# Kernel optimization log

Hardware: AMD Instinct MI355X
Metric: run time of the kernel (lower is better)

The kernel has to match this reference:

```python
import jax, jax.numpy as jnp
import numpy as np

BN_EPS = 1e-5


def trilinear_sample(feat, grid):
    """F.grid_sample 5D, mode='bilinear', padding_mode='border', align_corners=True.
    feat: (B,C,D,H,W); grid: (B,N,3) in [-1,1], last dim ordered (x,y,z) -> (W,H,D).
    Returns (B,N,C)."""
    B, C, D, H, W = feat.shape
    # align_corners=True unnormalization; border padding == clamp continuous coord
    x = jnp.clip((grid[..., 0] + 1.0) * 0.5 * (W - 1), 0.0, W - 1)
    y = jnp.clip((grid[..., 1] + 1.0) * 0.5 * (H - 1), 0.0, H - 1)
    z = jnp.clip((grid[..., 2] + 1.0) * 0.5 * (D - 1), 0.0, D - 1)
    x0 = jnp.floor(x).astype(jnp.int32); x1 = jnp.minimum(x0 + 1, W - 1)
    y0 = jnp.floor(y).astype(jnp.int32); y1 = jnp.minimum(y0 + 1, H - 1)
    z0 = jnp.floor(z).astype(jnp.int32); z1 = jnp.minimum(z0 + 1, D - 1)
    wx = (x - x0)[:, None, :]  # (B,1,N)
    wy = (y - y0)[:, None, :]
    wz = (z - z0)[:, None, :]
    flat = feat.reshape(B, C, D * H * W)

    def gather(zi, yi, xi):
        idx = (zi * H + yi) * W + xi            # (B,N)
        return jnp.take_along_axis(flat, idx[:, None, :], axis=2)  # (B,C,N)

    c00 = gather(z0, y0, x0) * (1 - wx) + gather(z0, y0, x1) * wx
    c01 = gather(z0, y1, x0) * (1 - wx) + gather(z0, y1, x1) * wx
    c10 = gather(z1, y0, x0) * (1 - wx) + gather(z1, y0, x1) * wx
    c11 = gather(z1, y1, x0) * (1 - wx) + gather(z1, y1, x1) * wx
    c0 = c00 * (1 - wy) + c01 * wy
    c1 = c10 * (1 - wy) + c11 * wy
    out = c0 * (1 - wz) + c1 * wz               # (B,C,N)
    return out.transpose(0, 2, 1)                # (B,N,C)


def batchnorm(x, gamma, beta, mean, var):
    # inference-mode BatchNorm1d over channel (last) dim
    return (x - mean) * jax.lax.rsqrt(var + BN_EPS) * gamma + beta


def setup_inputs() -> dict:
    key = jax.random.key(0)
    ks = jax.random.split(key, 16)
    B, C, D, H, W = 2, 128, 64, 64, 64
    N = 65536
    h1, h2 = 512, 512
    inp = {
        "dense_features": jax.random.normal(ks[0], (B, C, D, H, W), dtype=jnp.float32),
        "query_points": jax.random.uniform(ks[1], (B, N, 3), dtype=jnp.float32),
        "W1": jax.random.normal(ks[2], (C, h1), dtype=jnp.float32) / np.sqrt(C),
        "b1": jax.random.normal(ks[3], (h1,), dtype=jnp.float32) * 0.01,
        "g1": jax.random.uniform(ks[4], (h1,), dtype=jnp.float32, minval=0.5, maxval=1.5),
        "be1": jax.random.normal(ks[5], (h1,), dtype=jnp.float32) * 0.1,
        "m1": jax.random.normal(ks[6], (h1,), dtype=jnp.float32) * 0.1,
        "v1": jax.random.uniform(ks[7], (h1,), dtype=jnp.float32, minval=0.5, maxval=1.5),
        "W2": jax.random.normal(ks[8], (h1, h2), dtype=jnp.float32) / np.sqrt(h1),
        "b2": jax.random.normal(ks[9], (h2,), dtype=jnp.float32) * 0.01,
        "g2": jax.random.uniform(ks[10], (h2,), dtype=jnp.float32, minval=0.5, maxval=1.5),
        "be2": jax.random.normal(ks[11], (h2,), dtype=jnp.float32) * 0.1,
        "m2": jax.random.normal(ks[12], (h2,), dtype=jnp.float32) * 0.1,
        "v2": jax.random.uniform(ks[13], (h2,), dtype=jnp.float32, minval=0.5, maxval=1.5),
        "W3": jax.random.normal(ks[14], (h2, 1), dtype=jnp.float32) / np.sqrt(h2),
        "b3": jax.random.normal(ks[15], (1,), dtype=jnp.float32) * 0.01,
    }
    return inp


def reference(dense_features, query_points, W1, b1, g1, be1, m1, v1,
              W2, b2, g2, be2, m2, v2, W3, b3):
    grid = 2.0 * query_points - 1.0                       # (B,N,3)
    feats = trilinear_sample(dense_features, grid)        # (B,N,128)
    h = jax.nn.relu(batchnorm(jnp.einsum('bnc,ch->bnh', feats, W1) + b1, g1, be1, m1, v1))
    h = jax.nn.relu(batchnorm(jnp.einsum('bnc,ch->bnh', h, W2) + b2, g2, be2, m2, v2))
    out = jnp.einsum('bnc,ch->bnh', h, W3) + b3           # (B,N,1)
    return out
```

## Files before the change

### kernel.cpp

```cpp
#include <hip/hip_runtime.h>
#include <hip/hip_bf16.h>

using bf16x8 = __attribute__((ext_vector_type(8))) short;
using f32x4  = __attribute__((ext_vector_type(4))) float;
typedef unsigned short u16;
typedef unsigned int u32;

#define NB    2
#define NC    128
#define NPTS  65536
#define MTOT  (NB*NPTS)

static __device__ __forceinline__ u16 f2bf(float f) {
    u32 u = __float_as_uint(f);
    u32 r = (u + 0x7FFFu + ((u >> 16) & 1u)) >> 16;
    return (u16)r;
}
static __device__ __forceinline__ float bflo(u32 d) { return __uint_as_float(d << 16); }
static __device__ __forceinline__ float bfhi(u32 d) { return __uint_as_float(d & 0xFFFF0000u); }

__global__ void prep_kernel(
    const float* __restrict__ W1, const float* __restrict__ W2,
    const float* __restrict__ b1, const float* __restrict__ g1, const float* __restrict__ be1,
    const float* __restrict__ m1, const float* __restrict__ v1,
    const float* __restrict__ b2, const float* __restrict__ g2, const float* __restrict__ be2,
    const float* __restrict__ m2, const float* __restrict__ v2,
    u16* __restrict__ W1p, u16* __restrict__ W2p,
    float* __restrict__ s1, float* __restrict__ t1,
    float* __restrict__ s2, float* __restrict__ t2)
{
    int id = blockIdx.x * 256 + threadIdx.x;
    {
        int l = id & 63, nf = (id >> 6) & 7, kk = (id >> 9) & 15, t = id >> 13;
        int n  = t * 128 + nf * 16 + (l & 15);
        int c0 = kk * 32 + (l >> 4) * 8;
        #pragma unroll
        for (int j = 0; j < 8; ++j)
            W2p[id * 8 + j] = f2bf(W2[(size_t)(c0 + j) * 512 + n]);
    }
    if (id < 8192) {
        int l = id & 63, nf = (id >> 6) & 7, kk = (id >> 9) & 3, t = id >> 11;
        int n  = t * 128 + nf * 16 + (l & 15);
        int c0 = kk * 32 + (l >> 4) * 8;
        #pragma unroll
        for (int j = 0; j < 8; ++j)
            W1p[id * 8 + j] = f2bf(W1[(size_t)(c0 + j) * 512 + n]);
    }
    if (id < 512) {
        float s = g1[id] * rsqrtf(v1[id] + 1e-5f);
        s1[id] = s;
        t1[id] = (b1[id] - m1[id]) * s + be1[id];
        float ss = g2[id] * rsqrtf(v2[id] + 1e-5f);
        s2[id] = ss;
        t2[id] = (b2[id] - m2[id]) * ss + be2[id];
    }
}

__global__ __launch_bounds__(256) void transpose_kernel(const float* __restrict__ feat,
                                                        u16* __restrict__ featT)
{
    __shared__ float tile[128][33];
    int blk = blockIdx.x;
    int b   = blk >> 13;
    int v0  = (blk & 8191) << 5;
    int t   = threadIdx.x;
    int vi  = t & 31;
    int c0  = t >> 5;
    const float* fb = feat + ((size_t)b << 25);
    #pragma unroll
    for (int r = 0; r < 16; ++r) {
        int c = c0 + 8 * r;
        tile[c][vi] = fb[((size_t)c << 18) + v0 + vi];
    }
    __syncthreads();
    u32* outp = (u32*)(featT + (((size_t)b << 18) + v0) * 128);
    #pragma unroll
    for (int r = 0; r < 8; ++r) {
        int w  = t + 256 * r;
        int v  = w >> 6;
        int cp = w & 63;
        float lo = tile[2 * cp][v], hi = tile[2 * cp + 1][v];
        outp[w] = (u32)f2bf(lo) | ((u32)f2bf(hi) << 16);
    }
}

__global__ __launch_bounds__(256) void sampleT_kernel(const u16* __restrict__ featT,
                                                      const float* __restrict__ qp,
                                                      u16* __restrict__ fo)
{
    int tid = blockIdx.x * 256 + threadIdx.x;
    int p   = tid >> 6;
    int cp  = tid & 63;
    int b   = p >> 16;

    float qx = qp[p * 3 + 0];
    float qy = qp[p * 3 + 1];
    float qz = qp[p * 3 + 2];
    float x = fminf(fmaxf(qx * 63.0f, 0.0f), 63.0f);
    float y = fminf(fmaxf(qy * 63.0f, 0.0f), 63.0f);
    float z = fminf(fmaxf(qz * 63.0f, 0.0f), 63.0f);
    int x0 = (int)floorf(x), y0 = (int)floorf(y), z0 = (int)floorf(z);
    int x1 = min(x0 + 1, 63), y1 = min(y0 + 1, 63), z1 = min(z0 + 1, 63);
    float wx = x - (float)x0, wy = y - (float)y0, wz = z - (float)z0;

    const u32* fb = (const u32*)featT + (((size_t)b << 18) << 6);
    int zy00 = z0 * 4096 + y0 * 64, zy01 = z0 * 4096 + y1 * 64;
    int zy10 = z1 * 4096 + y0 * 64, zy11 = z1 * 4096 + y1 * 64;
    u32 d000 = fb[(size_t)(zy00 + x0) * 64 + cp];
    u32 d001 = fb[(size_t)(zy00 + x1) * 64 + cp];
    u32 d010 = fb[(size_t)(zy01 + x0) * 64 + cp];
    u32 d011 = fb[(size_t)(zy01 + x1) * 64 + cp];
    u32 d100 = fb[(size_t)(zy10 + x0) * 64 + cp];
    u32 d101 = fb[(size_t)(zy10 + x1) * 64 + cp];
    u32 d110 = fb[(size_t)(zy11 + x0) * 64 + cp];
    u32 d111 = fb[(size_t)(zy11 + x1) * 64 + cp];

    float omx = 1.0f - wx, omy = 1.0f - wy, omz = 1.0f - wz;
    float rl, rh;
    {
        float c00 = bflo(d000) * omx + bflo(d001) * wx;
        float c01 = bflo(d010) * omx + bflo(d011) * wx;
        float c10 = bflo(d100) * omx + bflo(d101) * wx;
        float c11 = bflo(d110) * omx + bflo(d111) * wx;
        rl = (c00 * omy + c01 * wy) * omz + (c10 * omy + c11 * wy) * wz;
    }
    {
        float c00 = bfhi(d000) * omx + bfhi(d001) * wx;
        float c01 = bfhi(d010) * omx + bfhi(d011) * wx;
        float c10 = bfhi(d100) * omx + bfhi(d101) * wx;
        float c11 = bfhi(d110) * omx + bfhi(d111) * wx;
        rh = (c00 * omy + c01 * wy) * omz + (c10 * omy + c11 * wy) * wz;
    }
    ((u32*)fo)[(size_t)p * 64 + cp] = (u32)f2bf(rl) | ((u32)f2bf(rh) << 16);
}

__global__ __launch_bounds__(256, 2) void mlp_kernel(
    const u16* __restrict__ feats, const u16* __restrict__ W1p, const u16* __restrict__ W2p,
    const float* __restrict__ s1, const float* __restrict__ t1,
    const float* __restrict__ s2, const float* __restrict__ t2,
    const float* __restrict__ W3, const float* __restrict__ b3,
    float* __restrict__ out)
{
    __shared__ u16 h1[64 * 512];
    __shared__ float outb[256];

    const int tidx = threadIdx.x;
    const int w    = tidx >> 6;
    const int l    = tidx & 63;
    const int l15  = l & 15;
    const int lq   = l >> 4;
    const int m0   = blockIdx.x * 64;
    const int n0   = w * 128;

    const u16* B1 = W1p + (size_t)(w * 4)  * 8 * 512;
    const u16* B2 = W2p + (size_t)(w * 16) * 8 * 512;

#define LOADA1(dst, kk) { _Pragma("unroll") for (int mf = 0; mf < 4; ++mf) \
    (dst)[mf] = *(const bf16x8*)(feats + (size_t)(m0 + mf * 16 + l15) * 128 + (kk) * 32 + lq * 8); }
#define LOADB1(dst, kk) { _Pragma("unroll") for (int nf = 0; nf < 8; ++nf) \
    (dst)[nf] = *(const bf16x8*)(B1 + ((kk) * 8 + nf) * 512 + l * 8); }
#define LOADB2(dst, kk) { _Pragma("unroll") for (int nf = 0; nf < 8; ++nf) \
    (dst)[nf] = *(const bf16x8*)(B2 + ((kk) * 8 + nf) * 512 + l * 8); }
#define LOADA2(dst, kk) { _Pragma("unroll") for (int mf = 0; mf < 4; ++mf) { \
    int row = mf * 16 + l15; \
    (dst)[mf] = *(const bf16x8*)(h1 + row * 512 + (((kk) * 32 + lq * 8) ^ ((row & 7) << 3))); } }

    f32x4 acc[4][8];
    #pragma unroll
    for (int i = 0; i < 4; ++i)
        #pragma unroll
        for (int j = 0; j < 8; ++j) acc[i][j] = (f32x4){0.f, 0.f, 0.f, 0.f};

    {
        bf16x8 a[2][4], b[2][8];
        LOADA1(a[0], 0); LOADB1(b[0], 0);
        #pragma unroll
        for (int kk = 0; kk < 4; ++kk) {
            const int cur = kk & 1, nxt = cur ^ 1;
            if (kk < 3) { LOADA1(a[nxt], kk + 1); LOADB1(b[nxt], kk + 1); }
            __builtin_amdgcn_s_setprio(1);
            #pragma unroll
            for (int mf = 0; mf < 4; ++mf)
                #pragma unroll
                for (int nf = 0; nf < 8; ++nf)
                    acc[mf][nf] = __builtin_amdgcn_mfma_f32_16x16x32_bf16(a[cur][mf], b[cur][nf], acc[mf][nf], 0, 0, 0);
            __builtin_amdgcn_s_setprio(0);
        }
    }

    bf16x8 pb[2][8];
    LOADB2(pb[0], 0);

    {
        float s1v[8], t1v[8];
        #pragma unroll
        for (int nf = 0; nf < 8; ++nf) {
            int col = n0 + nf * 16 + l15;
            s1v[nf] = s1[col]; t1v[nf] = t1[col];
        }
        #pragma unroll
        for (int mf = 0; mf < 4; ++mf)
            #pragma unroll
            for (int nf = 0; nf < 8; ++nf) {
                int col = n0 + nf * 16 + l15;
                #pragma unroll
                for (int i = 0; i < 4; ++i) {
                    int row = mf * 16 + lq * 4 + i;
                    float v = fmaxf(acc[mf][nf][i] * s1v[nf] + t1v[nf], 0.0f);
                    h1[row * 512 + (col ^ ((row & 7) << 3))] = f2bf(v);
                }
            }
    }
    __syncthreads();

    f32x4 acc2[4][8];
    #pragma unroll
    for (int i = 0; i < 4; ++i)
        #pragma unroll
        for (int j = 0; j < 8; ++j) acc2[i][j] = (f32x4){0.f, 0.f, 0.f, 0.f};

    #pragma unroll
    for (int kk = 0; kk < 16; ++kk) {
        const int cur = kk & 1, nxt = cur ^ 1;
        if (kk < 15) LOADB2(pb[nxt], kk + 1);
        bf16x8 a2[4];
        LOADA2(a2, kk);
        __builtin_amdgcn_s_setprio(1);
        #pragma unroll
        for (int mf = 0; mf < 4; ++mf)
            #pragma unroll
            for (int nf = 0; nf < 8; ++nf)
                acc2[mf][nf] = __builtin_amdgcn_mfma_f32_16x16x32_bf16(a2[mf], pb[cur][nf], acc2[mf][nf], 0, 0, 0);
        __builtin_amdgcn_s_setprio(0);
    }

    float part[16];
    #pragma unroll
    for (int i = 0; i < 16; ++i) part[i] = 0.f;
    {
        float s2v[8], t2v[8], w3v[8];
        #pragma unroll
        for (int nf = 0; nf < 8; ++nf) {
            int col = n0 + nf * 16 + l15;
            s2v[nf] = s2[col]; t2v[nf] = t2[col]; w3v[nf] = W3[col];
        }
        #pragma unroll
        for (int mf = 0; mf < 4; ++mf)
            #pragma unroll
            for (int nf = 0; nf < 8; ++nf)
                #pragma unroll
                for (int i = 0; i < 4; ++i) {
                    float h = fmaxf(acc2[mf][nf][i] * s2v[nf] + t2v[nf], 0.0f);
                    part[mf * 4 + i] += h * w3v[nf];
                }
    }
    #pragma unroll
    for (int off = 1; off < 16; off <<= 1)
        #pragma unroll
        for (int i = 0; i < 16; ++i) part[i] += __shfl_xor(part[i], off, 64);

    if (l15 == 0) {
        #pragma unroll
        for (int mf = 0; mf < 4; ++mf)
            #pragma unroll
            for (int i = 0; i < 4; ++i)
                outb[w * 64 + mf * 16 + lq * 4 + i] = part[mf * 4 + i];
    }
    __syncthreads();
    if (tidx < 64) {
        float r = outb[tidx] + outb[64 + tidx] + outb[128 + tidx] + outb[192 + tidx] + b3[0];
        out[m0 + tidx] = r;
    }
#undef LOADA1
#undef LOADB1
#undef LOADB2
#undef LOADA2
}

__global__ void sample_kernel(const float* __restrict__ feat,
                              const float* __restrict__ qp,
                              u16* __restrict__ fo)
{
    int tid = blockIdx.x * 256 + threadIdx.x;
    int p = tid >> 7;
    int c = tid & 127;
    int b = p >> 16;

    float qx = qp[p * 3 + 0], qy = qp[p * 3 + 1], qz = qp[p * 3 + 2];
    float x = fminf(fmaxf(qx * 63.0f, 0.0f), 63.0f);
    float y = fminf(fmaxf(qy * 63.0f, 0.0f), 63.0f);
    float z = fminf(fmaxf(qz * 63.0f, 0.0f), 63.0f);
    int x0 = (int)floorf(x), y0 = (int)floorf(y), z0 = (int)floorf(z);
    int x1 = min(x0 + 1, 63), y1 = min(y0 + 1, 63), z1 = min(z0 + 1, 63);
    float wx = x - (float)x0, wy = y - (float)y0, wz = z - (float)z0;

    const float* fb = feat + ((size_t)(b * NC + c) << 18);
    int zy00 = z0 * 4096 + y0 * 64, zy01 = z0 * 4096 + y1 * 64;
    int zy10 = z1 * 4096 + y0 * 64, zy11 = z1 * 4096 + y1 * 64;
    float f000 = fb[zy00 + x0], f001 = fb[zy00 + x1];
    float f010 = fb[zy01 + x0], f011 = fb[zy01 + x1];
    float f100 = fb[zy10 + x0], f101 = fb[zy10 + x1];
    float f110 = fb[zy11 + x0], f111 = fb[zy11 + x1];

    float omx = 1.0f - wx;
    float c00 = f000 * omx + f001 * wx;
    float c01 = f010 * omx + f011 * wx;
    float c10 = f100 * omx + f101 * wx;
    float c11 = f110 * omx + f111 * wx;
    float omy = 1.0f - wy;
    float c0 = c00 * omy + c01 * wy;
    float c1 = c10 * omy + c11 * wy;
    float v  = c0 * (1.0f - wz) + c1 * wz;
    fo[(size_t)p * 128 + c] = f2bf(v);
}

extern "C" void kernel_launch(void* const* d_in, const int* in_sizes, int n_in,
                              void* d_out, int out_size, void* d_ws, size_t ws_size,
                              hipStream_t stream)
{
    const float* feat = (const float*)d_in[0];
    const float* qp   = (const float*)d_in[1];
    const float* W1   = (const float*)d_in[2];
    const float* b1   = (const float*)d_in[3];
    const float* g1   = (const float*)d_in[4];
    const float* be1  = (const float*)d_in[5];
    const float* m1   = (const float*)d_in[6];
    const float* v1   = (const float*)d_in[7];
    const float* W2   = (const float*)d_in[8];
    const float* b2   = (const float*)d_in[9];
    const float* g2   = (const float*)d_in[10];
    const float* be2  = (const float*)d_in[11];
    const float* m2   = (const float*)d_in[12];
    const float* v2   = (const float*)d_in[13];
    const float* W3   = (const float*)d_in[14];
    const float* b3   = (const float*)d_in[15];

    char* ws = (char*)d_ws;
    u16*   W1p   = (u16*)(ws);
    u16*   W2p   = (u16*)(ws + 131072);
    float* s1    = (float*)(ws + 655360);
    float* t1    = (float*)(ws + 657408);
    float* s2    = (float*)(ws + 659456);
    float* t2    = (float*)(ws + 661504);
    u16*   feats = (u16*)(ws + 663552);
    u16*   featT = (u16*)(ws + 663552 + 33554432);
    const size_t needed = 663552 + 33554432 + 134217728;

    prep_kernel<<<128, 256, 0, stream>>>(W1, W2, b1, g1, be1, m1, v1,
                                         b2, g2, be2, m2, v2,
                                         W1p, W2p, s1, t1, s2, t2);
    if (ws_size >= needed) {
        transpose_kernel<<<16384, 256, 0, stream>>>(feat, featT);
        sampleT_kernel<<<(MTOT * 64) / 256, 256, 0, stream>>>(featT, qp, feats);
    } else {
        sample_kernel<<<(MTOT * 128) / 256, 256, 0, stream>>>(feat, qp, feats);
    }
    mlp_kernel<<<MTOT / 64, 256, 0, stream>>>(feats, W1p, W2p, s1, t1, s2, t2,
                                              W3, b3, (float*)d_out);
}
```

Before: 205.3 us.

## Vectorize trilinear gather loads and make MLP kernel persistent with A prefetch

```diff
diff --git a/kernel.cpp b/kernel.cpp
--- a/kernel.cpp
+++ b/kernel.cpp
@@ -3,6 +3,7 @@
 
 using bf16x8 = __attribute__((ext_vector_type(8))) short;
 using f32x4  = __attribute__((ext_vector_type(4))) float;
+using u32x4  = __attribute__((ext_vector_type(4))) unsigned int;
 typedef unsigned short u16;
 typedef unsigned int u32;
 
@@ -10,6 +11,8 @@
 #define NC    128
 #define NPTS  65536
 #define MTOT  (NB*NPTS)
+#define NTILE (MTOT/64)
+#define NBLK  512
 
 static __device__ __forceinline__ u16 f2bf(float f) {
     u32 u = __float_as_uint(f);
@@ -89,8 +92,8 @@
                                                       u16* __restrict__ fo)
 {
     int tid = blockIdx.x * 256 + threadIdx.x;
-    int p   = tid >> 6;
-    int cp  = tid & 63;
+    int p   = tid >> 4;
+    int li  = tid & 15;
     int b   = p >> 16;
 
     float qx = qp[p * 3 + 0];
@@ -103,35 +106,36 @@
     int x1 = min(x0 + 1, 63), y1 = min(y0 + 1, 63), z1 = min(z0 + 1, 63);
     float wx = x - (float)x0, wy = y - (float)y0, wz = z - (float)z0;
 
-    const u32* fb = (const u32*)featT + (((size_t)b << 18) << 6);
+    const u32* fb = (const u32*)featT + ((size_t)b << 24);
     int zy00 = z0 * 4096 + y0 * 64, zy01 = z0 * 4096 + y1 * 64;
     int zy10 = z1 * 4096 + y0 * 64, zy11 = z1 * 4096 + y1 * 64;
-    u32 d000 = fb[(size_t)(zy00 + x0) * 64 + cp];
-    u32 d001 = fb[(size_t)(zy00 + x1) * 64 + cp];
-    u32 d010 = fb[(size_t)(zy01 + x0) * 64 + cp];
-    u32 d011 = fb[(size_t)(zy01 + x1) * 64 + cp];
-    u32 d100 = fb[(size_t)(zy10 + x0) * 64 + cp];
-    u32 d101 = fb[(size_t)(zy10 + x1) * 64 + cp];
-    u32 d110 = fb[(size_t)(zy11 + x0) * 64 + cp];
-    u32 d111 = fb[(size_t)(zy11 + x1) * 64 + cp];
+    int co = li * 4;
+    u32x4 d000 = *(const u32x4*)(fb + (size_t)(zy00 + x0) * 64 + co);
+    u32x4 d001 = *(const u32x4*)(fb + (size_t)(zy00 + x1) * 64 + co);
+    u32x4 d010 = *(const u32x4*)(fb + (size_t)(zy01 + x0) * 64 + co);
+    u32x4 d011 = *(const u32x4*)(fb + (size_t)(zy01 + x1) * 64 + co);
+    u32x4 d100 = *(const u32x4*)(fb + (size_t)(zy10 + x0) * 64 + co);
+    u32x4 d101 = *(const u32x4*)(fb + (size_t)(zy10 + x1) * 64 + co);
+    u32x4 d110 = *(const u32x4*)(fb + (size_t)(zy11 + x0) * 64 + co);
+    u32x4 d111 = *(const u32x4*)(fb + (size_t)(zy11 + x1) * 64 + co);
 
     float omx = 1.0f - wx, omy = 1.0f - wy, omz = 1.0f - wz;
-    float rl, rh;
-    {
-        float c00 = bflo(d000) * omx + bflo(d001) * wx;
-        float c01 = bflo(d010) * omx + bflo(d011) * wx;
-        float c10 = bflo(d100) * omx + bflo(d101) * wx;
-        float c11 = bflo(d110) * omx + bflo(d111) * wx;
-        rl = (c00 * omy + c01 * wy) * omz + (c10 * omy + c11 * wy) * wz;
-    }
-    {
-        float c00 = bfhi(d000) * omx + bfhi(d001) * wx;
-        float c01 = bfhi(d010) * omx + bfhi(d011) * wx;
-        float c10 = bfhi(d100) * omx + bfhi(d101) * wx;
-        float c11 = bfhi(d110) * omx + bfhi(d111) * wx;
-        rh = (c00 * omy + c01 * wy) * omz + (c10 * omy + c11 * wy) * wz;
-    }
-    ((u32*)fo)[(size_t)p * 64 + cp] = (u32)f2bf(rl) | ((u32)f2bf(rh) << 16);
+    u32x4 o;
+    #pragma unroll
+    for (int j = 0; j < 4; ++j) {
+        float c00 = bflo(d000[j]) * omx + bflo(d001[j]) * wx;
+        float c01 = bflo(d010[j]) * omx + bflo(d011[j]) * wx;
+        float c10 = bflo(d100[j]) * omx + bflo(d101[j]) * wx;
+        float c11 = bflo(d110[j]) * omx + bflo(d111[j]) * wx;
+        float rl  = (c00 * omy + c01 * wy) * omz + (c10 * omy + c11 * wy) * wz;
+        float d00 = bfhi(d000[j]) * omx + bfhi(d001[j]) * wx;
+        float d01 = bfhi(d010[j]) * omx + bfhi(d011[j]) * wx;
+        float d10 = bfhi(d100[j]) * omx + bfhi(d101[j]) * wx;
+        float d11 = bfhi(d110[j]) * omx + bfhi(d111[j]) * wx;
+        float rh  = (d00 * omy + d01 * wy) * omz + (d10 * omy + d11 * wy) * wz;
+        o[j] = (u32)f2bf(rl) | ((u32)f2bf(rh) << 16);
+    }
+    *(u32x4*)((u32*)fo + (size_t)p * 64 + co) = o;
 }
 
 __global__ __launch_bounds__(256, 2) void mlp_kernel(
@@ -149,14 +153,13 @@
     const int l    = tidx & 63;
     const int l15  = l & 15;
     const int lq   = l >> 4;
-    const int m0   = blockIdx.x * 64;
     const int n0   = w * 128;
 
     const u16* B1 = W1p + (size_t)(w * 4)  * 8 * 512;
     const u16* B2 = W2p + (size_t)(w * 16) * 8 * 512;
 
-#define LOADA1(dst, kk) { _Pragma("unroll") for (int mf = 0; mf < 4; ++mf) \
-    (dst)[mf] = *(const bf16x8*)(feats + (size_t)(m0 + mf * 16 + l15) * 128 + (kk) * 32 + lq * 8); }
+#define LOADA1(dst, kk, m0v) { _Pragma("unroll") for (int mf = 0; mf < 4; ++mf) \
+    (dst)[mf] = *(const bf16x8*)(feats + (size_t)((m0v) + mf * 16 + l15) * 128 + (kk) * 32 + lq * 8); }
 #define LOADB1(dst, kk) { _Pragma("unroll") for (int nf = 0; nf < 8; ++nf) \
     (dst)[nf] = *(const bf16x8*)(B1 + ((kk) * 8 + nf) * 512 + l * 8); }
 #define LOADB2(dst, kk) { _Pragma("unroll") for (int nf = 0; nf < 8; ++nf) \
@@ -165,111 +168,123 @@
     int row = mf * 16 + l15; \
     (dst)[mf] = *(const bf16x8*)(h1 + row * 512 + (((kk) * 32 + lq * 8) ^ ((row & 7) << 3))); } }
 
-    f32x4 acc[4][8];
-    #pragma unroll
-    for (int i = 0; i < 4; ++i)
-        #pragma unroll
-        for (int j = 0; j < 8; ++j) acc[i][j] = (f32x4){0.f, 0.f, 0.f, 0.f};
-
-    {
-        bf16x8 a[2][4], b[2][8];
-        LOADA1(a[0], 0); LOADB1(b[0], 0);
-        #pragma unroll
-        for (int kk = 0; kk < 4; ++kk) {
-            const int cur = kk & 1, nxt = cur ^ 1;
-            if (kk < 3) { LOADA1(a[nxt], kk + 1); LOADB1(b[nxt], kk + 1); }
-            __builtin_amdgcn_s_setprio(1);
-            #pragma unroll
-            for (int mf = 0; mf < 4; ++mf)
-                #pragma unroll
-                for (int nf = 0; nf < 8; ++nf)
-                    acc[mf][nf] = __builtin_amdgcn_mfma_f32_16x16x32_bf16(a[cur][mf], b[cur][nf], acc[mf][nf], 0, 0, 0);
-            __builtin_amdgcn_s_setprio(0);
-        }
-    }
-
-    bf16x8 pb[2][8];
-    LOADB2(pb[0], 0);
-
-    {
-        float s1v[8], t1v[8];
-        #pragma unroll
-        for (int nf = 0; nf < 8; ++nf) {
-            int col = n0 + nf * 16 + l15;
-            s1v[nf] = s1[col]; t1v[nf] = t1[col];
-        }
-        #pragma unroll
-        for (int mf = 0; mf < 4; ++mf)
+    bf16x8 a1pre[4];
+    LOADA1(a1pre, 0, blockIdx.x * 64);
+
+    for (int t = blockIdx.x; t < NTILE; t += NBLK) {
+        const int m0 = t * 64;
+
+        f32x4 acc[4][8];
+        #pragma unroll
+        for (int i = 0; i < 4; ++i)
+            #pragma unroll
+            for (int j = 0; j < 8; ++j) acc[i][j] = (f32x4){0.f, 0.f, 0.f, 0.f};
+        {
+            bf16x8 av[2][4], bv[2][8];
+            #pragma unroll
+            for (int mf = 0; mf < 4; ++mf) av[0][mf] = a1pre[mf];
+            LOADB1(bv[0], 0);
+            #pragma unroll
+            for (int kk = 0; kk < 4; ++kk) {
+                const int cur = kk & 1, nxt = cur ^ 1;
+                if (kk < 3) { LOADA1(av[nxt], kk + 1, m0); LOADB1(bv[nxt], kk + 1); }
+                __builtin_amdgcn_s_setprio(1);
+                #pragma unroll
+                for (int mf = 0; mf < 4; ++mf)
+                    #pragma unroll
+                    for (int nf = 0; nf < 8; ++nf)
+                        acc[mf][nf] = __builtin_amdgcn_mfma_f32_16x16x32_bf16(av[cur][mf], bv[cur][nf], acc[mf][nf], 0, 0, 0);
+                __builtin_amdgcn_s_setprio(0);
+            }
+        }
+
+        bf16x8 pb[2][8];
+        LOADB2(pb[0], 0);
+
+        __syncthreads();
+
+        {
+            float s1v[8], t1v[8];
             #pragma unroll
             for (int nf = 0; nf < 8; ++nf) {
                 int col = n0 + nf * 16 + l15;
-                #pragma unroll
-                for (int i = 0; i < 4; ++i) {
-                    int row = mf * 16 + lq * 4 + i;
-                    float v = fmaxf(acc[mf][nf][i] * s1v[nf] + t1v[nf], 0.0f);
-                    h1[row * 512 + (col ^ ((row & 7) << 3))] = f2bf(v);
+                s1v[nf] = s1[col]; t1v[nf] = t1[col];
+            }
+            #pragma unroll
+            for (int mf = 0; mf < 4; ++mf)
+                #pragma unroll
+                for (int nf = 0; nf < 8; ++nf) {
+                    int col = n0 + nf * 16 + l15;
+                    #pragma unroll
+                    for (int i = 0; i < 4; ++i) {
+                        int row = mf * 16 + lq * 4 + i;
+                        float v = fmaxf(acc[mf][nf][i] * s1v[nf] + t1v[nf], 0.0f);
+                        h1[row * 512 + (col ^ ((row & 7) << 3))] = f2bf(v);
+                    }
                 }
+        }
+        __syncthreads();
+
+        f32x4 acc2[4][8];
+        #pragma unroll
+        for (int i = 0; i < 4; ++i)
+            #pragma unroll
+            for (int j = 0; j < 8; ++j) acc2[i][j] = (f32x4){0.f, 0.f, 0.f, 0.f};
+
+        #pragma unroll
+        for (int kk = 0; kk < 16; ++kk) {
+            const int cur = kk & 1, nxt = cur ^ 1;
+            if (kk < 15) LOADB2(pb[nxt], kk + 1);
+            bf16x8 a2[4];
+            LOADA2(a2, kk);
+            __builtin_amdgcn_s_setprio(1);
+            #pragma unroll
+            for (int mf = 0; mf < 4; ++mf)
+                #pragma unroll
+                for (int nf = 0; nf < 8; ++nf)
+                    acc2[mf][nf] = __builtin_amdgcn_mfma_f32_16x16x32_bf16(a2[mf], pb[cur][nf], acc2[mf][nf], 0, 0, 0);
+            __builtin_amdgcn_s_setprio(0);
+        }
+
+        if (t + NBLK < NTILE) { LOADA1(a1pre, 0, m0 + NBLK * 64); }
+
+        float part[16];
+        #pragma unroll
+        for (int i = 0; i < 16; ++i) part[i] = 0.f;
+        {
+            float s2v[8], t2v[8], w3v[8];
+            #pragma unroll
+            for (int nf = 0; nf < 8; ++nf) {
+                int col = n0 + nf * 16 + l15;
+                s2v[nf] = s2[col]; t2v[nf] = t2[col]; w3v[nf] = W3[col];
             }
-    }
-    __syncthreads();
-
-    f32x4 acc2[4][8];
-    #pragma unroll
-    for (int i = 0; i < 4; ++i)
-        #pragma unroll
-        for (int j = 0; j < 8; ++j) acc2[i][j] = (f32x4){0.f, 0.f, 0.f, 0.f};
-
-    #pragma unroll
-    for (int kk = 0; kk < 16; ++kk) {
-        const int cur = kk & 1, nxt = cur ^ 1;
-        if (kk < 15) LOADB2(pb[nxt], kk + 1);
-        bf16x8 a2[4];
-        LOADA2(a2, kk);
-        __builtin_amdgcn_s_setprio(1);
-        #pragma unroll
-        for (int mf = 0; mf < 4; ++mf)
-            #pragma unroll
-            for (int nf = 0; nf < 8; ++nf)
-                acc2[mf][nf] = __builtin_amdgcn_mfma_f32_16x16x32_bf16(a2[mf], pb[cur][nf], acc2[mf][nf], 0, 0, 0);
-        __builtin_amdgcn_s_setprio(0);
-    }
-
-    float part[16];
-    #pragma unroll
-    for (int i = 0; i < 16; ++i) part[i] = 0.f;
-    {
-        float s2v[8], t2v[8], w3v[8];
-        #pragma unroll
-        for (int nf = 0; nf < 8; ++nf) {
-            int col = n0 + nf * 16 + l15;
-            s2v[nf] = s2[col]; t2v[nf] = t2[col]; w3v[nf] = W3[col];
-        }
-        #pragma unroll
-        for (int mf = 0; mf < 4; ++mf)
-            #pragma unroll
-            for (int nf = 0; nf < 8; ++nf)
-                #pragma unroll
-                for (int i = 0; i < 4; ++i) {
-                    float h = fmaxf(acc2[mf][nf][i] * s2v[nf] + t2v[nf], 0.0f);
-                    part[mf * 4 + i] += h * w3v[nf];
-                }
-    }
-    #pragma unroll
-    for (int off = 1; off < 16; off <<= 1)
-        #pragma unroll
-        for (int i = 0; i < 16; ++i) part[i] += __shfl_xor(part[i], off, 64);
-
-    if (l15 == 0) {
-        #pragma unroll
-        for (int mf = 0; mf < 4; ++mf)
-            #pragma unroll
-            for (int i = 0; i < 4; ++i)
-                outb[w * 64 + mf * 16 + lq * 4 + i] = part[mf * 4 + i];
-    }
-    __syncthreads();
-    if (tidx < 64) {
-        float r = outb[tidx] + outb[64 + tidx] + outb[128 + tidx] + outb[192 + tidx] + b3[0];
-        out[m0 + tidx] = r;
+            #pragma unroll
+            for (int mf = 0; mf < 4; ++mf)
+                #pragma unroll
+                for (int nf = 0; nf < 8; ++nf)
+                    #pragma unroll
+                    for (int i = 0; i < 4; ++i) {
+                        float h = fmaxf(acc2[mf][nf][i] * s2v[nf] + t2v[nf], 0.0f);
+                        part[mf * 4 + i] += h * w3v[nf];
+                    }
+        }
+        #pragma unroll
+        for (int off = 1; off < 16; off <<= 1)
+            #pragma unroll
+            for (int i = 0; i < 16; ++i) part[i] += __shfl_xor(part[i], off, 64);
+
+        if (l15 == 0) {
+            #pragma unroll
+            for (int mf = 0; mf < 4; ++mf)
+                #pragma unroll
+                for (int i = 0; i < 4; ++i)
+                    outb[w * 64 + mf * 16 + lq * 4 + i] = part[mf * 4 + i];
+        }
+        __syncthreads();
+        if (tidx < 64) {
+            float r = outb[tidx] + outb[64 + tidx] + outb[128 + tidx] + outb[192 + tidx] + b3[0];
+            out[m0 + tidx] = r;
+        }
     }
 #undef LOADA1
 #undef LOADB1
@@ -351,10 +366,10 @@
                                          W1p, W2p, s1, t1, s2, t2);
     if (ws_size >= needed) {
         transpose_kernel<<<16384, 256, 0, stream>>>(feat, featT);
-        sampleT_kernel<<<(MTOT * 64) / 256, 256, 0, stream>>>(featT, qp, feats);
+        sampleT_kernel<<<(MTOT * 16) / 256, 256, 0, stream>>>(featT, qp, feats);
     } else {
         sample_kernel<<<(MTOT * 128) / 256, 256, 0, stream>>>(feat, qp, feats);
     }
-    mlp_kernel<<<MTOT / 64, 256, 0, stream>>>(feats, W1p, W2p, s1, t1, s2, t2,
-                                              W3, b3, (float*)d_out);
-}
+    mlp_kernel<<<NBLK, 256, 0, stream>>>(feats, W1p, W2p, s1, t1, s2, t2,
+                                         W3, b3, (float*)d_out);
+}
```

After: 798.8 us. 289% more time.
